# Performance work log

Hardware: AMD Instinct MI355X
Metric: run time of the kernel (lower is better)

The kernel has to match this reference:

```python
import jax, jax.numpy as jnp
import numpy as np

EPS = 1e-05
K = 32


def _knn_idx(xyz_B3N, k):
    # negative squared pairwise distance: -||xi||^2 + 2 xi.xj - ||xj||^2
    inner = 2.0 * jnp.einsum('bdn,bdm->bnm', xyz_B3N, xyz_B3N)  # [B,N,N]
    xx = jnp.sum(xyz_B3N ** 2, axis=1)  # [B,N]
    pd = inner - xx[:, :, None] - xx[:, None, :]
    _, idx = jax.lax.top_k(pd, k)  # [B,N,k] nearest (largest negative dist)
    return idx


def setup_inputs() -> dict:
    key = jax.random.key(0)
    k1, k2 = jax.random.split(key)
    B, N, C = 16, 4096, 64
    xyz_B3N = jax.random.normal(k1, (B, 3, N), dtype=jnp.float32)
    feats_BNC = jax.random.normal(k2, (B, N, C), dtype=jnp.float32)
    alpha = jnp.ones((C,), dtype=jnp.float32)
    beta = jnp.zeros((C,), dtype=jnp.float32)
    return {"xyz_B3N": xyz_B3N, "feats_BNC": feats_BNC, "alpha": alpha, "beta": beta}


def reference(xyz_B3N, feats_BNC, alpha, beta):
    idx = _knn_idx(xyz_B3N, K)  # [B,N,k]
    # gather neighbor features directly: [B,N,k,C]
    neigh = jax.vmap(lambda f, i: f[i])(feats_BNC, idx)
    offset = neigh - feats_BNC[:, :, None, :]  # [B,N,k,C]
    sigma = jnp.mean(offset ** 2)  # global scalar
    gaed = (offset / (sigma + EPS)) * alpha + beta
    pooled = jnp.max(gaed, axis=2)  # [B,N,C]
    return pooled
```

## Files before the change

### kernel.cpp

```cpp
#include <hip/hip_runtime.h>
#include <float.h>

#define BB 16
#define NN 4096
#define CC 64
#define KNN 32
#define NSLICE 16
#define SSZ 256
#define CKEEP 8
#define NQ 65536


#define M3 __builtin_amdgcn_fmed3f

__device__ __forceinline__ int lane_rank(unsigned long long m) {
    return __builtin_amdgcn_mbcnt_hi((unsigned)(m >> 32),
           __builtin_amdgcn_mbcnt_lo((unsigned)m, 0u));
}

#define CHAIN8 \
  h07=M3(pd,h07,h06); h06=M3(pd,h06,h05); h05=M3(pd,h05,h04); \
  h04=M3(pd,h04,h03); h03=M3(pd,h03,h02); h02=M3(pd,h02,h01); \
  h01=M3(pd,h01,h00); h00=fmaxf(h00,pd);

#define H8_DECL \
  float h00=-FLT_MAX,h01=-FLT_MAX,h02=-FLT_MAX,h03=-FLT_MAX, \
        h04=-FLT_MAX,h05=-FLT_MAX,h06=-FLT_MAX,h07=-FLT_MAX;

__global__ __launch_bounds__(256) void prep_kernel(
        const float* __restrict__ xyz, float4* __restrict__ pts4,
        int* __restrict__ flag_cnt) {
#pragma clang fp contract(off)
    const int p = blockIdx.x * 256 + threadIdx.x;
    if (p == 0) flag_cnt[0] = 0;
    const int b = p >> 12;
    const int i = p & (NN - 1);
    const float* xb = xyz + (size_t)b * (3 * NN);
    float x = xb[i], y = xb[NN + i], z = xb[2 * NN + i];
    float xx = ((x * x) + (y * y)) + (z * z);
    pts4[p] = make_float4(x, y, z, xx);
}

__global__ __launch_bounds__(256) void knn_select_kernel(
        const float4* __restrict__ pts4, float* __restrict__ val_buf) {
#pragma clang fp contract(off)
    __shared__ float4 pts[SSZ];
    const int tid = threadIdx.x;
    const int blk = blockIdx.x;
    const int s = blk & 15;
    const int g = (blk >> 4) & 15;
    const int b = blk >> 8;
    const float4* pb = pts4 + (b << 12);

    pts[tid] = pb[(s << 8) | tid];
    const int q = (g << 8) | tid;
    const float4 qp = pb[q];
    const float qx = qp.x, qy = qp.y, qz = qp.z, qxx = qp.w;
    __syncthreads();

    H8_DECL
#pragma unroll 4
    for (int j = 0; j < SSZ; ++j) {
        float4 cp = pts[j];
        float dot = __builtin_fmaf(qz, cp.z, __builtin_fmaf(qy, cp.y, qx * cp.x));
        float pd = ((dot + dot) - qxx) - cp.w;
        CHAIN8
    }

    const int qg = (b << 12) | q;
    float* vp = val_buf + (size_t)(s * CKEEP) * NQ + qg;
#define ST(t, ht) vp[(size_t)(t) * NQ] = ht;
    ST(0,h00) ST(1,h01) ST(2,h02) ST(3,h03)
    ST(4,h04) ST(5,h05) ST(6,h06) ST(7,h07)
#undef ST
}

__global__ __launch_bounds__(64) void knn_merge_kernel(
        const float* __restrict__ val_buf, float* __restrict__ T_buf,
        int* __restrict__ pack_buf, int* __restrict__ flag_list,
        int* __restrict__ flag_cnt) {
    __shared__ float lv[64 * 129];
    const int tid = threadIdx.x;
    const int qg = blockIdx.x * 64 + tid;
    float* my = lv + tid * 129;
    for (int t = 0; t < 128; ++t) my[t] = val_buf[(size_t)t * NQ + qg];

    int p0=0,p1=0,p2=0,p3=0,p4=0,p5=0,p6=0,p7=0,
        p8=0,p9=0,p10=0,p11=0,p12=0,p13=0,p14=0,p15=0;
    float v0 =my[0],  v1 =my[8],  v2 =my[16],  v3 =my[24];
    float v4 =my[32], v5 =my[40], v6 =my[48],  v7 =my[56];
    float v8 =my[64], v9 =my[72], v10=my[80],  v11=my[88];
    float v12=my[96], v13=my[104],v14=my[112], v15=my[120];
    float T = -FLT_MAX;
    for (int step = 0; step < 32; ++step) {
        float best = v0; int bp = 0;
        if (v1  > best) { best = v1;  bp = 1; }
        if (v2  > best) { best = v2;  bp = 2; }
        if (v3  > best) { best = v3;  bp = 3; }
        if (v4  > best) { best = v4;  bp = 4; }
        if (v5  > best) { best = v5;  bp = 5; }
        if (v6  > best) { best = v6;  bp = 6; }
        if (v7  > best) { best = v7;  bp = 7; }
        if (v8  > best) { best = v8;  bp = 8; }
        if (v9  > best) { best = v9;  bp = 9; }
        if (v10 > best) { best = v10; bp = 10; }
        if (v11 > best) { best = v11; bp = 11; }
        if (v12 > best) { best = v12; bp = 12; }
        if (v13 > best) { best = v13; bp = 13; }
        if (v14 > best) { best = v14; bp = 14; }
        if (v15 > best) { best = v15; bp = 15; }
        T = best;
        if      (bp==0)  { ++p0;  v0  = (p0 <8)?my[p0]      :-FLT_MAX; }
        else if (bp==1)  { ++p1;  v1  = (p1 <8)?my[8+p1]    :-FLT_MAX; }
        else if (bp==2)  { ++p2;  v2  = (p2 <8)?my[16+p2]   :-FLT_MAX; }
        else if (bp==3)  { ++p3;  v3  = (p3 <8)?my[24+p3]   :-FLT_MAX; }
        else if (bp==4)  { ++p4;  v4  = (p4 <8)?my[32+p4]   :-FLT_MAX; }
        else if (bp==5)  { ++p5;  v5  = (p5 <8)?my[40+p5]   :-FLT_MAX; }
        else if (bp==6)  { ++p6;  v6  = (p6 <8)?my[48+p6]   :-FLT_MAX; }
        else if (bp==7)  { ++p7;  v7  = (p7 <8)?my[56+p7]   :-FLT_MAX; }
        else if (bp==8)  { ++p8;  v8  = (p8 <8)?my[64+p8]   :-FLT_MAX; }
        else if (bp==9)  { ++p9;  v9  = (p9 <8)?my[72+p9]   :-FLT_MAX; }
        else if (bp==10) { ++p10; v10 = (p10<8)?my[80+p10]  :-FLT_MAX; }
        else if (bp==11) { ++p11; v11 = (p11<8)?my[88+p11]  :-FLT_MAX; }
        else if (bp==12) { ++p12; v12 = (p12<8)?my[96+p12]  :-FLT_MAX; }
        else if (bp==13) { ++p13; v13 = (p13<8)?my[104+p13] :-FLT_MAX; }
        else if (bp==14) { ++p14; v14 = (p14<8)?my[112+p14] :-FLT_MAX; }
        else             { ++p15; v15 = (p15<8)?my[120+p15] :-FLT_MAX; }
    }

    int gt = 0, eq = 0;
    bool flag = false;
    for (int sl = 0; sl < 16; ++sl) {
        const int base = sl * 8;
        for (int t = 0; t < 8; ++t) {
            float v = my[base + t];
            gt += (v > T); eq += (v == T);
        }
        flag = flag || (my[base + 7] >= T);
    }

    T_buf[qg] = T;
    if (flag) {
        int pos = atomicAdd(flag_cnt, 1);
        flag_list[pos] = qg;
    }
    const int budget = min(eq, 32 - gt);
    pack_buf[qg] = gt | (budget << 16);
}

__global__ __launch_bounds__(256) void knn_fallback_kernel(
        const float* __restrict__ xyz, const int* __restrict__ flag_list,
        const int* __restrict__ flag_cnt, float* __restrict__ T_buf,
        int* __restrict__ pack_buf) {
#pragma clang fp contract(off)
    const int nflag = flag_cnt[0];
    const int lane = threadIdx.x & 63;
    const int wid = (blockIdx.x * 256 + threadIdx.x) >> 6;
    const int nw = (gridDim.x * 256) >> 6;
    for (int w = wid; w < nflag; w += nw) {
        const int qg = flag_list[w];
        const int b = qg >> 12;
        const int q = qg & (NN - 1);
        const float* xb = xyz + (size_t)b * (3 * NN);
        const float qx = xb[q], qy = xb[NN + q], qz = xb[2 * NN + q];
        const float qxx = ((qx * qx) + (qy * qy)) + (qz * qz);

        unsigned key[64];
#pragma unroll
        for (int i = 0; i < 64; ++i) {
            const int j = (i << 6) | lane;
            float x = xb[j], y = xb[NN + j], z = xb[2 * NN + j];
            float xxc = ((x * x) + (y * y)) + (z * z);
            float dot = __builtin_fmaf(qz, z, __builtin_fmaf(qy, y, qx * x));
            float pd = ((dot + dot) - qxx) - xxc;
            unsigned u = __float_as_uint(pd);
            key[i] = u ^ ((u >> 31) ? 0xFFFFFFFFu : 0x80000000u);
        }

        unsigned cur = 0u;
        for (int bit = 31; bit >= 0; --bit) {
            const unsigned cand = cur | (1u << bit);
            int c = 0;
#pragma unroll
            for (int i = 0; i < 64; ++i) c += (key[i] >= cand) ? 1 : 0;
#pragma unroll
            for (int o = 32; o >= 1; o >>= 1) c += __shfl_xor(c, o, 64);
            if (c >= 32) cur = cand;
        }
        const float T = __uint_as_float(
            (cur & 0x80000000u) ? (cur ^ 0x80000000u) : ~cur);

        int ge = 0;
#pragma unroll
        for (int i = 0; i < 64; ++i) {
            ge += (key[i] > cur) ? 1 : 0;
            ge += (key[i] == cur) ? 0x10000 : 0;
        }
#pragma unroll
        for (int o = 32; o >= 1; o >>= 1) ge += __shfl_xor(ge, o, 64);
        const int gt_total = ge & 0xFFFF;
        const int eq_total = ge >> 16;

        if (lane == 0) {
            T_buf[qg] = T;
            const int budget = min(eq_total, 32 - gt_total);
            pack_buf[qg] = gt_total | (budget << 16);
        }
    }
}

__global__ __launch_bounds__(512) void knn_emit_kernel(
        const float4* __restrict__ pts4, const float* __restrict__ T_buf,
        const int* __restrict__ pack_buf, int* __restrict__ idx_out) {
#pragma clang fp contract(off)
    __shared__ float4 chunk[1024];
    const int tid = threadIdx.x;
    const int lane = tid & 63;
    const int qg = (blockIdx.x << 3) | (tid >> 6);
    const int b = qg >> 12;
    const float4* pb = pts4 + (b << 12);
    const float4 qp = pb[qg & (NN - 1)];
    const float qx = qp.x, qy = qp.y, qz = qp.z, qxx = qp.w;
    const float T = T_buf[qg];
    const int pk = pack_buf[qg];
    const int g_total = pk & 0xFFFF;
    const int budget = pk >> 16;
    int* outp = idx_out + (size_t)qg * KNN;
    int slot = 0, neq = 0;

    for (int c = 0; c < 4; ++c) {
        __syncthreads();
        chunk[tid] = pb[(c << 10) | tid];
        chunk[tid + 512] = pb[(c << 10) | (tid + 512)];
        __syncthreads();
#pragma unroll 4
        for (int j = 0; j < 16; ++j) {
            const int il = (j << 6) | lane;
            float4 cp = chunk[il];
            float dot = __builtin_fmaf(qz, cp.z, __builtin_fmaf(qy, cp.y, qx * cp.x));
            float pd = ((dot + dot) - qxx) - cp.w;
            const bool gt = pd > T;
            const bool eq = pd == T;
            const unsigned long long mgt = __ballot(gt);
            const unsigned long long meq = __ballot(eq);
            if (gt) outp[slot + lane_rank(mgt)] = (c << 10) | il;
            if (eq) {
                const int r = neq + lane_rank(meq);
                if (r < budget) outp[g_total + r] = (c << 10) | il;
            }
            slot += __builtin_popcountll(mgt);
            neq += __builtin_popcountll(meq);
        }
    }
}

__global__ __launch_bounds__(256) void gather_minmax_kernel(
        const float* __restrict__ feats, const int* __restrict__ idx_in,
        float* __restrict__ mx_buf, float* __restrict__ mn_buf,
        double* __restrict__ partials) {
    const int tid = threadIdx.x;
    const int w = tid >> 6;
    const int lane = tid & 63;
    const int q = blockIdx.x * 4 + w;
    const int b = q >> 12;
    const float* fb = feats + (size_t)b * (NN * CC);
    const float center = feats[(size_t)q * CC + lane];
    const int* ip = idx_in + (size_t)q * KNN;

    float mx = -FLT_MAX, mn = FLT_MAX;
    double ss = 0.0;
#pragma unroll 4
    for (int k = 0; k < KNN; ++k) {
        int nb = ip[k];
        float v = fb[(size_t)nb * CC + lane];
        float off = v - center;
        mx = fmaxf(mx, off);
        mn = fminf(mn, off);
        double od = (double)off;
        ss = fma(od, od, ss);
    }
    mx_buf[(size_t)q * CC + lane] = mx;
    mn_buf[(size_t)q * CC + lane] = mn;

#pragma unroll
    for (int o = 32; o >= 1; o >>= 1) ss += __shfl_down(ss, o, 64);
    __shared__ double wsum[4];
    if (lane == 0) wsum[w] = ss;
    __syncthreads();
    if (tid == 0) partials[blockIdx.x] = (wsum[0] + wsum[1]) + (wsum[2] + wsum[3]);
}

__global__ __launch_bounds__(256) void sigma_kernel(const double* __restrict__ partials,
                                                    float* __restrict__ sigma) {
    __shared__ double red[256];
    double s = 0.0;
    for (int i = threadIdx.x; i < 16384; i += 256) s += partials[i];
    red[threadIdx.x] = s;
    __syncthreads();
    for (int o = 128; o >= 1; o >>= 1) {
        if (threadIdx.x < o) red[threadIdx.x] += red[threadIdx.x + o];
        __syncthreads();
    }
    if (threadIdx.x == 0) sigma[0] = (float)(red[0] * (1.0 / 134217728.0));
}

__global__ __launch_bounds__(256) void finalize_kernel(
        const float* __restrict__ mx_buf, const float* __restrict__ mn_buf,
        const float* __restrict__ alpha, const float* __restrict__ beta,
        const float* __restrict__ sigma, float* __restrict__ out) {
#pragma clang fp contract(off)
    const int e = blockIdx.x * 256 + threadIdx.x;
    const int c = e & (CC - 1);
    const float s = sigma[0] + 1e-5f;
    const float a = alpha[c];
    const float bt = beta[c];
    const float off = (a >= 0.f) ? mx_buf[e] : mn_buf[e];
    const float t = off / s;
    out[e] = (t * a) + bt;
}

extern "C" void kernel_launch(void* const* d_in, const int* in_sizes, int n_in,
                              void* d_out, int out_size, void* d_ws, size_t ws_size,
                              hipStream_t stream) {
    (void)in_sizes; (void)n_in; (void)out_size; (void)ws_size;
    const float* xyz   = (const float*)d_in[0];
    const float* feats = (const float*)d_in[1];
    const float* alpha = (const float*)d_in[2];
    const float* beta  = (const float*)d_in[3];
    float* out = (float*)d_out;

    char* ws = (char*)d_ws;
    float*  val_buf  = (float*)ws;
    int*    idx_buf  = (int*)ws;
    float*  mx_buf   = (float*)(ws + 8388608);
    float*  mn_buf   = (float*)(ws + 25165824);
    int*    flag_list= (int*)(ws + 33554432);
    int*    flag_cnt = (int*)(ws + 33816576);
    float4* pts4     = (float4*)(ws + 34078720);
    float*  T_buf    = (float*)(ws + 41943040);
    int*    pack_buf = (int*)(ws + 42205184);
    double* partials = (double*)(ws + 41943040);
    float*  sigma    = (float*)(ws + 42074112);

    prep_kernel<<<NQ / 256, 256, 0, stream>>>(xyz, pts4, flag_cnt);
    knn_select_kernel<<<BB * 16 * NSLICE, 256, 0, stream>>>(pts4, val_buf);
    knn_merge_kernel<<<NQ / 64, 64, 0, stream>>>(val_buf, T_buf, pack_buf,
                                                 flag_list, flag_cnt);
    knn_fallback_kernel<<<256, 256, 0, stream>>>(xyz, flag_list, flag_cnt,
                                                 T_buf, pack_buf);
    knn_emit_kernel<<<NQ / 8, 512, 0, stream>>>(pts4, T_buf, pack_buf, idx_buf);
    gather_minmax_kernel<<<NQ / 4, 256, 0, stream>>>(feats, idx_buf, mx_buf,
                                                     mn_buf, partials);
    sigma_kernel<<<1, 256, 0, stream>>>(partials, sigma);
    finalize_kernel<<<(NQ * CC) / 256, 256, 0, stream>>>(mx_buf, mn_buf, alpha,
                                                         beta, sigma, out);
}
```

Baseline: 385.3 us.

## Pack candidate index into sort keys and drop the KNN emit pass

The select kernel now builds monotone unsigned keys whose low 12 bits encode the candidate index, keeping the top 8 per slice with integer med3. The merge kernel can then write the 32 neighbour indices directly, and the separate emit kernel that recomputed all N distances per query is removed. Queries whose 32nd and 33rd keys share truncated distance bits, or whose slices may have overflowed, go to the fallback, which now also emits indices itself. This trades distance precision in the low mantissa bits for skipping a full N×N distance pass, and relies on the fallback to keep tie handling exact. Workspace buffers are re-laid out to match.

```diff
diff --git a/kernel.cpp b/kernel.cpp
--- a/kernel.cpp
+++ b/kernel.cpp
@@ -11,21 +11,21 @@
 #define NQ 65536
 
 
-#define M3 __builtin_amdgcn_fmed3f
-
 __device__ __forceinline__ int lane_rank(unsigned long long m) {
     return __builtin_amdgcn_mbcnt_hi((unsigned)(m >> 32),
            __builtin_amdgcn_mbcnt_lo((unsigned)m, 0u));
 }
 
-#define CHAIN8 \
-  h07=M3(pd,h07,h06); h06=M3(pd,h06,h05); h05=M3(pd,h05,h04); \
-  h04=M3(pd,h04,h03); h03=M3(pd,h03,h02); h02=M3(pd,h02,h01); \
-  h01=M3(pd,h01,h00); h00=fmaxf(h00,pd);
-
-#define H8_DECL \
-  float h00=-FLT_MAX,h01=-FLT_MAX,h02=-FLT_MAX,h03=-FLT_MAX, \
-        h04=-FLT_MAX,h05=-FLT_MAX,h06=-FLT_MAX,h07=-FLT_MAX;
+__device__ __forceinline__ unsigned med3u(unsigned a, unsigned b, unsigned c) {
+    unsigned d;
+    asm("v_med3_u32 %0, %1, %2, %3" : "=v"(d) : "v"(a), "v"(b), "v"(c));
+    return d;
+}
+
+#define UCHAIN8 \
+  h07=med3u(ky,h07,h06); h06=med3u(ky,h06,h05); h05=med3u(ky,h05,h04); \
+  h04=med3u(ky,h04,h03); h03=med3u(ky,h03,h02); h02=med3u(ky,h02,h01); \
+  h01=med3u(ky,h01,h00); h00=(h00>ky)?h00:ky;
 
 __global__ __launch_bounds__(256) void prep_kernel(
         const float* __restrict__ xyz, float4* __restrict__ pts4,
@@ -42,7 +42,7 @@
 }
 
 __global__ __launch_bounds__(256) void knn_select_kernel(
-        const float4* __restrict__ pts4, float* __restrict__ val_buf) {
+        const float4* __restrict__ pts4, unsigned* __restrict__ val_buf) {
 #pragma clang fp contract(off)
     __shared__ float4 pts[SSZ];
     const int tid = threadIdx.x;
@@ -55,20 +55,25 @@
     pts[tid] = pb[(s << 8) | tid];
     const int q = (g << 8) | tid;
     const float4 qp = pb[q];
-    const float qx = qp.x, qy = qp.y, qz = qp.z, qxx = qp.w;
+    const float qx = qp.x, qy = qp.y, qz = qp.z;
+    const float nqxx = -qp.w;
     __syncthreads();
 
-    H8_DECL
+    unsigned h00=0,h01=0,h02=0,h03=0,h04=0,h05=0,h06=0,h07=0;
+    const unsigned ibase = 4095u - (unsigned)(s << 8);
 #pragma unroll 4
     for (int j = 0; j < SSZ; ++j) {
         float4 cp = pts[j];
         float dot = __builtin_fmaf(qz, cp.z, __builtin_fmaf(qy, cp.y, qx * cp.x));
-        float pd = ((dot + dot) - qxx) - cp.w;
-        CHAIN8
+        float pd = __builtin_fmaf(2.0f, dot, nqxx) - cp.w;
+        unsigned u = __float_as_uint(pd);
+        unsigned mono = u ^ (unsigned)(((int)u >> 31) | 0x80000000);
+        unsigned ky = (mono & 0xFFFFF000u) | (ibase - (unsigned)j);
+        UCHAIN8
     }
 
     const int qg = (b << 12) | q;
-    float* vp = val_buf + (size_t)(s * CKEEP) * NQ + qg;
+    unsigned* vp = val_buf + (size_t)(s * CKEEP) * NQ + qg;
 #define ST(t, ht) vp[(size_t)(t) * NQ] = ht;
     ST(0,h00) ST(1,h01) ST(2,h02) ST(3,h03)
     ST(4,h04) ST(5,h05) ST(6,h06) ST(7,h07)
@@ -76,24 +81,24 @@
 }
 
 __global__ __launch_bounds__(64) void knn_merge_kernel(
-        const float* __restrict__ val_buf, float* __restrict__ T_buf,
-        int* __restrict__ pack_buf, int* __restrict__ flag_list,
-        int* __restrict__ flag_cnt) {
-    __shared__ float lv[64 * 129];
+        const unsigned* __restrict__ val_buf, int* __restrict__ idx_out,
+        int* __restrict__ flag_list, int* __restrict__ flag_cnt) {
+    __shared__ unsigned lv[64 * 129];
     const int tid = threadIdx.x;
     const int qg = blockIdx.x * 64 + tid;
-    float* my = lv + tid * 129;
+    unsigned* my = lv + tid * 129;
     for (int t = 0; t < 128; ++t) my[t] = val_buf[(size_t)t * NQ + qg];
 
     int p0=0,p1=0,p2=0,p3=0,p4=0,p5=0,p6=0,p7=0,
         p8=0,p9=0,p10=0,p11=0,p12=0,p13=0,p14=0,p15=0;
-    float v0 =my[0],  v1 =my[8],  v2 =my[16],  v3 =my[24];
-    float v4 =my[32], v5 =my[40], v6 =my[48],  v7 =my[56];
-    float v8 =my[64], v9 =my[72], v10=my[80],  v11=my[88];
-    float v12=my[96], v13=my[104],v14=my[112], v15=my[120];
-    float T = -FLT_MAX;
-    for (int step = 0; step < 32; ++step) {
-        float best = v0; int bp = 0;
+    unsigned v0 =my[0],  v1 =my[8],  v2 =my[16],  v3 =my[24];
+    unsigned v4 =my[32], v5 =my[40], v6 =my[48],  v7 =my[56];
+    unsigned v8 =my[64], v9 =my[72], v10=my[80],  v11=my[88];
+    unsigned v12=my[96], v13=my[104],v14=my[112], v15=my[120];
+    int* outp = idx_out + (size_t)qg * KNN;
+    unsigned key32 = 0u, key33 = 0u;
+    for (int step = 0; step < 33; ++step) {
+        unsigned best = v0; int bp = 0;
         if (v1  > best) { best = v1;  bp = 1; }
         if (v2  > best) { best = v2;  bp = 2; }
         if (v3  > best) { best = v3;  bp = 3; }
@@ -109,49 +114,39 @@
         if (v13 > best) { best = v13; bp = 13; }
         if (v14 > best) { best = v14; bp = 14; }
         if (v15 > best) { best = v15; bp = 15; }
-        T = best;
-        if      (bp==0)  { ++p0;  v0  = (p0 <8)?my[p0]      :-FLT_MAX; }
-        else if (bp==1)  { ++p1;  v1  = (p1 <8)?my[8+p1]    :-FLT_MAX; }
-        else if (bp==2)  { ++p2;  v2  = (p2 <8)?my[16+p2]   :-FLT_MAX; }
-        else if (bp==3)  { ++p3;  v3  = (p3 <8)?my[24+p3]   :-FLT_MAX; }
-        else if (bp==4)  { ++p4;  v4  = (p4 <8)?my[32+p4]   :-FLT_MAX; }
-        else if (bp==5)  { ++p5;  v5  = (p5 <8)?my[40+p5]   :-FLT_MAX; }
-        else if (bp==6)  { ++p6;  v6  = (p6 <8)?my[48+p6]   :-FLT_MAX; }
-        else if (bp==7)  { ++p7;  v7  = (p7 <8)?my[56+p7]   :-FLT_MAX; }
-        else if (bp==8)  { ++p8;  v8  = (p8 <8)?my[64+p8]   :-FLT_MAX; }
-        else if (bp==9)  { ++p9;  v9  = (p9 <8)?my[72+p9]   :-FLT_MAX; }
-        else if (bp==10) { ++p10; v10 = (p10<8)?my[80+p10]  :-FLT_MAX; }
-        else if (bp==11) { ++p11; v11 = (p11<8)?my[88+p11]  :-FLT_MAX; }
-        else if (bp==12) { ++p12; v12 = (p12<8)?my[96+p12]  :-FLT_MAX; }
-        else if (bp==13) { ++p13; v13 = (p13<8)?my[104+p13] :-FLT_MAX; }
-        else if (bp==14) { ++p14; v14 = (p14<8)?my[112+p14] :-FLT_MAX; }
-        else             { ++p15; v15 = (p15<8)?my[120+p15] :-FLT_MAX; }
-    }
-
-    int gt = 0, eq = 0;
-    bool flag = false;
-    for (int sl = 0; sl < 16; ++sl) {
-        const int base = sl * 8;
-        for (int t = 0; t < 8; ++t) {
-            float v = my[base + t];
-            gt += (v > T); eq += (v == T);
-        }
-        flag = flag || (my[base + 7] >= T);
-    }
-
-    T_buf[qg] = T;
+        if (step == 32) { key33 = best; break; }
+        outp[step] = 4095 - (int)(best & 4095u);
+        if (step == 31) key32 = best;
+        if      (bp==0)  { ++p0;  v0  = (p0 <8)?my[p0]      :0u; }
+        else if (bp==1)  { ++p1;  v1  = (p1 <8)?my[8+p1]    :0u; }
+        else if (bp==2)  { ++p2;  v2  = (p2 <8)?my[16+p2]   :0u; }
+        else if (bp==3)  { ++p3;  v3  = (p3 <8)?my[24+p3]   :0u; }
+        else if (bp==4)  { ++p4;  v4  = (p4 <8)?my[32+p4]   :0u; }
+        else if (bp==5)  { ++p5;  v5  = (p5 <8)?my[40+p5]   :0u; }
+        else if (bp==6)  { ++p6;  v6  = (p6 <8)?my[48+p6]   :0u; }
+        else if (bp==7)  { ++p7;  v7  = (p7 <8)?my[56+p7]   :0u; }
+        else if (bp==8)  { ++p8;  v8  = (p8 <8)?my[64+p8]   :0u; }
+        else if (bp==9)  { ++p9;  v9  = (p9 <8)?my[72+p9]   :0u; }
+        else if (bp==10) { ++p10; v10 = (p10<8)?my[80+p10]  :0u; }
+        else if (bp==11) { ++p11; v11 = (p11<8)?my[88+p11]  :0u; }
+        else if (bp==12) { ++p12; v12 = (p12<8)?my[96+p12]  :0u; }
+        else if (bp==13) { ++p13; v13 = (p13<8)?my[104+p13] :0u; }
+        else if (bp==14) { ++p14; v14 = (p14<8)?my[112+p14] :0u; }
+        else             { ++p15; v15 = (p15<8)?my[120+p15] :0u; }
+    }
+
+    bool flag = ((key32 >> 12) == (key33 >> 12));
+    for (int sl = 0; sl < 16; ++sl)
+        flag = flag || (my[sl * 8 + 7] >= key33);
     if (flag) {
         int pos = atomicAdd(flag_cnt, 1);
         flag_list[pos] = qg;
     }
-    const int budget = min(eq, 32 - gt);
-    pack_buf[qg] = gt | (budget << 16);
 }
 
 __global__ __launch_bounds__(256) void knn_fallback_kernel(
         const float* __restrict__ xyz, const int* __restrict__ flag_list,
-        const int* __restrict__ flag_cnt, float* __restrict__ T_buf,
-        int* __restrict__ pack_buf) {
+        const int* __restrict__ flag_cnt, int* __restrict__ idx_out) {
 #pragma clang fp contract(off)
     const int nflag = flag_cnt[0];
     const int lane = threadIdx.x & 63;
@@ -164,6 +159,7 @@
         const float* xb = xyz + (size_t)b * (3 * NN);
         const float qx = xb[q], qy = xb[NN + q], qz = xb[2 * NN + q];
         const float qxx = ((qx * qx) + (qy * qy)) + (qz * qz);
+        const float nqxx = -qxx;
 
         unsigned key[64];
 #pragma unroll
@@ -172,9 +168,9 @@
             float x = xb[j], y = xb[NN + j], z = xb[2 * NN + j];
             float xxc = ((x * x) + (y * y)) + (z * z);
             float dot = __builtin_fmaf(qz, z, __builtin_fmaf(qy, y, qx * x));
-            float pd = ((dot + dot) - qxx) - xxc;
+            float pd = __builtin_fmaf(2.0f, dot, nqxx) - xxc;
             unsigned u = __float_as_uint(pd);
-            key[i] = u ^ ((u >> 31) ? 0xFFFFFFFFu : 0x80000000u);
+            key[i] = u ^ (unsigned)(((int)u >> 31) | 0x80000000);
         }
 
         unsigned cur = 0u;
@@ -187,8 +183,6 @@
             for (int o = 32; o >= 1; o >>= 1) c += __shfl_xor(c, o, 64);
             if (c >= 32) cur = cand;
         }
-        const float T = __uint_as_float(
-            (cur & 0x80000000u) ? (cur ^ 0x80000000u) : ~cur);
 
         int ge = 0;
 #pragma unroll
@@ -199,54 +193,20 @@
 #pragma unroll
         for (int o = 32; o >= 1; o >>= 1) ge += __shfl_xor(ge, o, 64);
         const int gt_total = ge & 0xFFFF;
-        const int eq_total = ge >> 16;
-
-        if (lane == 0) {
-            T_buf[qg] = T;
-            const int budget = min(eq_total, 32 - gt_total);
-            pack_buf[qg] = gt_total | (budget << 16);
-        }
-    }
-}
-
-__global__ __launch_bounds__(512) void knn_emit_kernel(
-        const float4* __restrict__ pts4, const float* __restrict__ T_buf,
-        const int* __restrict__ pack_buf, int* __restrict__ idx_out) {
-#pragma clang fp contract(off)
-    __shared__ float4 chunk[1024];
-    const int tid = threadIdx.x;
-    const int lane = tid & 63;
-    const int qg = (blockIdx.x << 3) | (tid >> 6);
-    const int b = qg >> 12;
-    const float4* pb = pts4 + (b << 12);
-    const float4 qp = pb[qg & (NN - 1)];
-    const float qx = qp.x, qy = qp.y, qz = qp.z, qxx = qp.w;
-    const float T = T_buf[qg];
-    const int pk = pack_buf[qg];
-    const int g_total = pk & 0xFFFF;
-    const int budget = pk >> 16;
-    int* outp = idx_out + (size_t)qg * KNN;
-    int slot = 0, neq = 0;
-
-    for (int c = 0; c < 4; ++c) {
-        __syncthreads();
-        chunk[tid] = pb[(c << 10) | tid];
-        chunk[tid + 512] = pb[(c << 10) | (tid + 512)];
-        __syncthreads();
-#pragma unroll 4
-        for (int j = 0; j < 16; ++j) {
-            const int il = (j << 6) | lane;
-            float4 cp = chunk[il];
-            float dot = __builtin_fmaf(qz, cp.z, __builtin_fmaf(qy, cp.y, qx * cp.x));
-            float pd = ((dot + dot) - qxx) - cp.w;
-            const bool gt = pd > T;
-            const bool eq = pd == T;
-            const unsigned long long mgt = __ballot(gt);
-            const unsigned long long meq = __ballot(eq);
-            if (gt) outp[slot + lane_rank(mgt)] = (c << 10) | il;
-            if (eq) {
+        const int budget = min(ge >> 16, 32 - gt_total);
+
+        int* outp = idx_out + (size_t)qg * KNN;
+        int slot = 0, neq = 0;
+#pragma unroll
+        for (int i = 0; i < 64; ++i) {
+            const bool isgt = key[i] > cur;
+            const bool iseq = key[i] == cur;
+            const unsigned long long mgt = __ballot(isgt);
+            const unsigned long long meq = __ballot(iseq);
+            if (isgt) outp[slot + lane_rank(mgt)] = (i << 6) | lane;
+            if (iseq) {
                 const int r = neq + lane_rank(meq);
-                if (r < budget) outp[g_total + r] = (c << 10) | il;
+                if (r < budget) outp[gt_total + r] = (i << 6) | lane;
             }
             slot += __builtin_popcountll(mgt);
             neq += __builtin_popcountll(meq);
@@ -330,25 +290,22 @@
     float* out = (float*)d_out;
 
     char* ws = (char*)d_ws;
-    float*  val_buf  = (float*)ws;
-    int*    idx_buf  = (int*)ws;
-    float*  mx_buf   = (float*)(ws + 8388608);
-    float*  mn_buf   = (float*)(ws + 25165824);
-    int*    flag_list= (int*)(ws + 33554432);
-    int*    flag_cnt = (int*)(ws + 33816576);
-    float4* pts4     = (float4*)(ws + 34078720);
-    float*  T_buf    = (float*)(ws + 41943040);
-    int*    pack_buf = (int*)(ws + 42205184);
-    double* partials = (double*)(ws + 41943040);
-    float*  sigma    = (float*)(ws + 42074112);
+    unsigned* val_buf  = (unsigned*)ws;
+    float*    mx_buf   = (float*)ws;
+    float*    mn_buf   = (float*)(ws + 16777216);
+    int*      idx_buf  = (int*)(ws + 33554432);
+    int*      flag_list= (int*)(ws + 41943040);
+    int*      flag_cnt = (int*)(ws + 42205184);
+    float4*   pts4     = (float4*)(ws + 42205200);
+    double*   partials = (double*)(ws + 42205200);
+    float*    sigma    = (float*)(ws + 42336272);
 
     prep_kernel<<<NQ / 256, 256, 0, stream>>>(xyz, pts4, flag_cnt);
     knn_select_kernel<<<BB * 16 * NSLICE, 256, 0, stream>>>(pts4, val_buf);
-    knn_merge_kernel<<<NQ / 64, 64, 0, stream>>>(val_buf, T_buf, pack_buf,
+    knn_merge_kernel<<<NQ / 64, 64, 0, stream>>>(val_buf, idx_buf,
                                                  flag_list, flag_cnt);
     knn_fallback_kernel<<<256, 256, 0, stream>>>(xyz, flag_list, flag_cnt,
-                                                 T_buf, pack_buf);
-    knn_emit_kernel<<<NQ / 8, 512, 0, stream>>>(pts4, T_buf, pack_buf, idx_buf);
+                                                 idx_buf);
     gather_minmax_kernel<<<NQ / 4, 256, 0, stream>>>(feats, idx_buf, mx_buf,
                                                      mn_buf, partials);
     sigma_kernel<<<1, 256, 0, stream>>>(partials, sigma);
```

Result: faster. 348.9 us (-9.5%).
